# Kernel tuning notes

Hardware: AMD Instinct MI355X
Metric: run time of the kernel (lower is better)

Reference implementation:

```python
import jax, jax.numpy as jnp
import numpy as np

WIDTH = 8    # hwcfg['width']: bitstream code width, BinGen scale = 2**WIDTH
DEPTH = 12   # hwcfg['depth']: FSUAdd accumulator depth, bound = 2**DEPTH - 1


def setup_inputs() -> dict:
    key = jax.random.key(0)
    k1, k2 = jax.random.split(key)
    batch, in_f, out_f = 4096, 2048, 4096
    # stochastic-computing input: one bit per element for the current cycle
    x = jax.random.bernoulli(k1, 0.5, (batch, in_f)).astype(jnp.float32)
    # bipolar weight probabilities in [-1, 1] (weight_ext)
    w = jax.random.uniform(k2, (out_f, in_f), jnp.float32, -1.0, 1.0)
    # Sobol RNG sample for the current cycle, values live in [0, 2**WIDTH)
    rng_val = jnp.ones((1,), jnp.float32) * 128.0
    return {"input": x, "weight": w, "rng_val": rng_val}


def reference(input, weight, rng_val):
    """One cycle of FSUMatMul: static bipolar FSUMul + scaled bipolar FSUAdd (first cycle, acc=0)."""
    batch, in_f = input.shape
    # ---- FSUMul (static, bipolar) ----
    prob = (weight + 1.0) * 0.5                      # bipolar value -> unipolar probability
    source = jnp.round(prob * (2.0 ** WIDTH))        # BinGen: quantized binary source
    path = (source > rng_val[0]).astype(input.dtype)  # BSGen bit for each weight, (out, in)
    # product bit = XNOR(x, path) = 1 - |x - path| on {0,1} bits.
    # Sum over in_features of the (batch,out,in) broadcast product, computed exactly
    # via the GEMM identity: sum_k 1-|x-p| = in_f - (sum x + sum p - 2 * x @ p^T).
    sx = jnp.sum(input, axis=1)                      # (batch,)
    sp = jnp.sum(path, axis=1)                       # (out,)
    xp = jnp.einsum('bi,oi->bo', input, path)        # (batch, out) GEMM
    sum_prod = in_f - (sx[:, None] + sp[None, :] - 2.0 * xp)
    # ---- FSUAdd (bipolar, scaled: scale_carry = entry = in_f -> offset = 0) ----
    scale_carry = jnp.float32(in_f)
    acc = jnp.clip(sum_prod, 0.0, 2.0 ** DEPTH - 1)  # first-cycle accumulator state (init 0)
    out = (acc >= scale_carry).astype(jnp.float32)   # emitted output bit per (batch, out)
    return out
```

## Files before the change

kernel.cpp:

```cpp
#include <hip/hip_runtime.h>


#define BATCH 4096
#define INF   2048
#define OUTF  4096

__global__ __launch_bounds__(256) void pack0_kernel(
    const float* __restrict__ x, const float* __restrict__ w,
    const float* __restrict__ rng,
    unsigned long long* __restrict__ xp0, unsigned long long* __restrict__ pp0)
{
    const int lane = threadIdx.x & 63;
    const int wav  = threadIdx.x >> 6;
    const int id   = blockIdx.x * 4 + wav;

    if (id < BATCH) {
        const float v = x[(size_t)id * INF + lane];
        const unsigned long long b = __ballot(v != 0.0f);
        if (lane == 0) xp0[id] = b;
    } else {
        const int o = id - BATCH;
        const float v = w[(size_t)o * INF + lane];
        const float s = rintf((v + 1.0f) * 0.5f * 256.0f);
        const unsigned long long b = __ballot(s > rng[0]);
        if (lane == 0) pp0[o] = b;
    }
}

__global__ __launch_bounds__(256) void cmp_kernel(
    const unsigned long long* __restrict__ xp0,
    const unsigned long long* __restrict__ pp0,
    const float* __restrict__ x, const float* __restrict__ w,
    const float* __restrict__ rng,
    float* __restrict__ out)
{
    const int tid = threadIdx.x;
    const int o0  = (blockIdx.x * 256 + tid) * 4;
    const int b0  = blockIdx.y * 16;

    const unsigned long long p0 = pp0[o0 + 0];
    const unsigned long long p1 = pp0[o0 + 1];
    const unsigned long long p2 = pp0[o0 + 2];
    const unsigned long long p3 = pp0[o0 + 3];

    for (int i = 0; i < 16; ++i) {
        const int b = b0 + i;
        const unsigned long long xw = xp0[b];
        bool eq[4];
        eq[0] = (p0 == xw);
        eq[1] = (p1 == xw);
        eq[2] = (p2 == xw);
        eq[3] = (p3 == xw);
        if (eq[0] | eq[1] | eq[2] | eq[3]) {
            const float r = rng[0];
            for (int j = 0; j < 4; ++j) {
                if (!eq[j]) continue;
                const int o = o0 + j;
                bool all = true;
                for (int k = 64; k < INF; ++k) {
                    const bool xb = x[(size_t)b * INF + k] != 0.0f;
                    const bool pb =
                        rintf((w[(size_t)o * INF + k] + 1.0f) * 0.5f * 256.0f) > r;
                    all = all && (xb == pb);
                }
                eq[j] = all;
            }
        }
        float4 res = make_float4(eq[0] ? 1.0f : 0.0f, eq[1] ? 1.0f : 0.0f,
                                 eq[2] ? 1.0f : 0.0f, eq[3] ? 1.0f : 0.0f);
        *reinterpret_cast<float4*>(out + (size_t)b * OUTF + o0) = res;
    }
}

extern "C" void kernel_launch(void* const* d_in, const int* in_sizes, int n_in,
                              void* d_out, int out_size, void* d_ws, size_t ws_size,
                              hipStream_t stream) {
    const float* x   = (const float*)d_in[0];
    const float* w   = (const float*)d_in[1];
    const float* rng = (const float*)d_in[2];
    float* out = (float*)d_out;

    unsigned long long* xp0 = (unsigned long long*)d_ws;
    unsigned long long* pp0 = xp0 + BATCH;

    pack0_kernel<<<dim3((BATCH + OUTF) / 4), dim3(256), 0, stream>>>(
        x, w, rng, xp0, pp0);

    cmp_kernel<<<dim3(OUTF / 1024, BATCH / 16), dim3(256), 0, stream>>>(
        xp0, pp0, x, w, rng, out);
}
```

Before: 107.5 us.

## Fuse bit-packing into the compare kernel with shared-memory packed tiles

Merges the separate packing kernel and the compare kernel into one kernel. Each block packs the first 64 bits of its 1024 weight rows and 32 input rows into shared memory, then runs the same early-reject equality compare. Output stores become nontemporal. This removes a launch and the workspace round trip, but every block along the batch axis repacks the same weight rows, which adds redundant global/L2 reads and ballot work.

```diff
diff --git a/kernel.cpp b/kernel.cpp
--- a/kernel.cpp
+++ b/kernel.cpp
@@ -5,54 +5,64 @@
 #define INF   2048
 #define OUTF  4096
 
-__global__ __launch_bounds__(256) void pack0_kernel(
+#define BTILE 32
+#define OTILE 1024
+
+typedef float f4 __attribute__((ext_vector_type(4)));
+
+__global__ __launch_bounds__(256) void fsu_fused(
     const float* __restrict__ x, const float* __restrict__ w,
-    const float* __restrict__ rng,
-    unsigned long long* __restrict__ xp0, unsigned long long* __restrict__ pp0)
+    const float* __restrict__ rng, float* __restrict__ out)
 {
-    const int lane = threadIdx.x & 63;
-    const int wav  = threadIdx.x >> 6;
-    const int id   = blockIdx.x * 4 + wav;
+    __shared__ unsigned long long pp[OTILE];
+    __shared__ unsigned long long xq[BTILE];
 
-    if (id < BATCH) {
-        const float v = x[(size_t)id * INF + lane];
-        const unsigned long long b = __ballot(v != 0.0f);
-        if (lane == 0) xp0[id] = b;
-    } else {
-        const int o = id - BATCH;
-        const float v = w[(size_t)o * INF + lane];
-        const float s = rintf((v + 1.0f) * 0.5f * 256.0f);
-        const unsigned long long b = __ballot(s > rng[0]);
-        if (lane == 0) pp0[o] = b;
+    const int tid   = threadIdx.x;
+    const int lane  = tid & 63;
+    const int wav   = tid >> 6;
+    const int obase = blockIdx.x * OTILE;
+    const int bbase = blockIdx.y * BTILE;
+    const float r   = rng[0];
+
+    {
+        const int lr0 = wav * (OTILE / 4);
+        #pragma unroll 8
+        for (int t = 0; t < OTILE / 4; ++t) {
+            const int lr = lr0 + t;
+            const float v = w[(size_t)(obase + lr) * INF + lane];
+            const float s = rintf((v + 1.0f) * 0.5f * 256.0f);
+            const unsigned long long bb = __ballot(s > r);
+            if (lane == 0) pp[lr] = bb;
+        }
     }
-}
+    {
+        const int lb0 = wav * (BTILE / 4);
+        #pragma unroll
+        for (int t = 0; t < BTILE / 4; ++t) {
+            const int lb = lb0 + t;
+            const float v = x[(size_t)(bbase + lb) * INF + lane];
+            const unsigned long long bb = __ballot(v != 0.0f);
+            if (lane == 0) xq[lb] = bb;
+        }
+    }
+    __syncthreads();
 
-__global__ __launch_bounds__(256) void cmp_kernel(
-    const unsigned long long* __restrict__ xp0,
-    const unsigned long long* __restrict__ pp0,
-    const float* __restrict__ x, const float* __restrict__ w,
-    const float* __restrict__ rng,
-    float* __restrict__ out)
-{
-    const int tid = threadIdx.x;
-    const int o0  = (blockIdx.x * 256 + tid) * 4;
-    const int b0  = blockIdx.y * 16;
+    const int ol = tid * 4;
+    const unsigned long long p0 = pp[ol + 0];
+    const unsigned long long p1 = pp[ol + 1];
+    const unsigned long long p2 = pp[ol + 2];
+    const unsigned long long p3 = pp[ol + 3];
+    const int o0 = obase + ol;
 
-    const unsigned long long p0 = pp0[o0 + 0];
-    const unsigned long long p1 = pp0[o0 + 1];
-    const unsigned long long p2 = pp0[o0 + 2];
-    const unsigned long long p3 = pp0[o0 + 3];
-
-    for (int i = 0; i < 16; ++i) {
-        const int b = b0 + i;
-        const unsigned long long xw = xp0[b];
-        bool eq[4];
-        eq[0] = (p0 == xw);
-        eq[1] = (p1 == xw);
-        eq[2] = (p2 == xw);
-        eq[3] = (p3 == xw);
-        if (eq[0] | eq[1] | eq[2] | eq[3]) {
-            const float r = rng[0];
+    for (int i = 0; i < BTILE; ++i) {
+        const int b = bbase + i;
+        const unsigned long long xv = xq[i];
+        bool eq0 = (p0 == xv);
+        bool eq1 = (p1 == xv);
+        bool eq2 = (p2 == xv);
+        bool eq3 = (p3 == xv);
+        if (eq0 | eq1 | eq2 | eq3) {
+            bool eq[4] = {eq0, eq1, eq2, eq3};
             for (int j = 0; j < 4; ++j) {
                 if (!eq[j]) continue;
                 const int o = o0 + j;
@@ -65,10 +75,12 @@
                 }
                 eq[j] = all;
             }
+            eq0 = eq[0]; eq1 = eq[1]; eq2 = eq[2]; eq3 = eq[3];
         }
-        float4 res = make_float4(eq[0] ? 1.0f : 0.0f, eq[1] ? 1.0f : 0.0f,
-                                 eq[2] ? 1.0f : 0.0f, eq[3] ? 1.0f : 0.0f);
-        *reinterpret_cast<float4*>(out + (size_t)b * OUTF + o0) = res;
+        f4 res = { eq0 ? 1.0f : 0.0f, eq1 ? 1.0f : 0.0f,
+                   eq2 ? 1.0f : 0.0f, eq3 ? 1.0f : 0.0f };
+        __builtin_nontemporal_store(
+            res, reinterpret_cast<f4*>(out + (size_t)b * OUTF + o0));
     }
 }
 
@@ -80,12 +92,8 @@
     const float* rng = (const float*)d_in[2];
     float* out = (float*)d_out;
 
-    unsigned long long* xp0 = (unsigned long long*)d_ws;
-    unsigned long long* pp0 = xp0 + BATCH;
+    (void)d_ws; (void)ws_size;
 
-    pack0_kernel<<<dim3((BATCH + OUTF) / 4), dim3(256), 0, stream>>>(
-        x, w, rng, xp0, pp0);
-
-    cmp_kernel<<<dim3(OUTF / 1024, BATCH / 16), dim3(256), 0, stream>>>(
-        xp0, pp0, x, w, rng, out);
+    fsu_fused<<<dim3(OUTF / OTILE, BATCH / BTILE), dim3(256), 0, stream>>>(
+        x, w, rng, out);
 }
```

Result: slower. 199.9 us (+85.9%).
